# Optimization experiments

Hardware: AMD Instinct MI355X
Metric: run time of the kernel (lower is better)

The kernel has to match this reference:

```python
import jax, jax.numpy as jnp
import numpy as np


def setup_inputs() -> dict:
    key = jax.random.key(0)
    k1, k2 = jax.random.split(key)
    n, K = 1024, 8
    pred_y = jax.random.normal(k1, (n, K), dtype=jnp.float32)
    true_y = jax.random.randint(k2, (n, K), 0, 2).astype(jnp.int32)  # multi-label 0/1
    return {"pred_y": pred_y, "true_y": true_y}


def reference(pred_y, true_y):
    # mode == 'pairwise2':
    #   sum_{i,j} sum_{a: y[a,i]==1} sum_{b: y[b,j]==0} log(1 + exp(-(pred[a,i] - pred[b,j])))
    #   normalized by |S_pos| * |S_neg| (total counts over the whole label matrix).
    # The double class loop + cartesian_prod is exactly an all-pairs interaction
    # between flattened positive entries and flattened negative entries.
    pos = (true_y == 1)
    neg = (true_y == 0)
    v = pred_y.reshape(-1)                      # [n*K]
    mp = pos.reshape(-1).astype(pred_y.dtype)   # positive-entry mask
    mn = neg.reshape(-1).astype(pred_y.dtype)   # negative-entry mask
    # loss(p - q) = log(1 + exp(-(p - q))) = softplus(q - p)
    diff = v[None, :] - v[:, None]              # [nK, nK]; diff[a, b] = v_b - v_a
    sp = jax.nn.softplus(diff)
    total = jnp.sum(sp * (mp[:, None] * mn[None, :]))
    denom = jnp.sum(mp) * jnp.sum(mn)           # |S_pos| * |S_neg|
    return total / denom
```

## Files before the change

kernel.cpp:

```cpp
#include <hip/hip_runtime.h>

#define CBLK 256
#define GRID 1024
#define PBLK 512
#define RT   9

#define LOG2E 1.4426950408889634f
#define LN2   0.6931471805599453
#define BIGF  1.0e30f

__device__ __forceinline__ float fast_exp2(float x) {
#if __has_builtin(__builtin_amdgcn_exp2f)
    return __builtin_amdgcn_exp2f(x);
#else
    return exp2f(x);
#endif
}
__device__ __forceinline__ float fast_log2(float x) {
#if __has_builtin(__builtin_amdgcn_logf)
    return __builtin_amdgcn_logf(x);
#else
    return log2f(x);
#endif
}

__global__ void compact_kernel(const float* __restrict__ v,
                               const int* __restrict__ ty,
                               int* __restrict__ cnt,
                               float* __restrict__ vpos,
                               float* __restrict__ vneg,
                               int N) {
    const int i    = blockIdx.x * blockDim.x + threadIdx.x;
    const int lane = threadIdx.x & 63;

    const bool valid = (i < N);
    float val = 0.0f;
    int   t   = -1;
    if (valid) { val = v[i] * LOG2E; t = ty[i]; }

    const bool isP = valid && (t == 1);
    const bool isN = valid && (t == 0);

    const unsigned long long mp = __ballot(isP);
    const unsigned long long mn = __ballot(isN);
    const unsigned long long lt = (lane == 0) ? 0ull : (~0ull >> (64 - lane));

    int basep = 0, basen = 0;
    if (lane == 0) {
        basep = atomicAdd(&cnt[0], __popcll(mp));
        basen = atomicAdd(&cnt[1], __popcll(mn));
    }
    basep = __shfl(basep, 0, 64);
    basen = __shfl(basen, 0, 64);

    if (isP) vpos[basep + __popcll(mp & lt)] = val;
    if (isN) vneg[basen + __popcll(mn & lt)] = val;
}

__global__ __launch_bounds__(PBLK) void pair_kernel(
        const int* __restrict__ cnt,
        const float* __restrict__ vpos,
        const float* __restrict__ vneg,
        float* __restrict__ partials) {
    const int P   = cnt[0];
    const int Q   = cnt[1];
    const int tid = threadIdx.x;

    float accm = 0.0f;
    float accl = 0.0f;

    for (int base = 0; base < P; base += RT * PBLK) {
        float pa[RT];
        #pragma unroll
        for (int r = 0; r < RT; ++r) {
            const int idx = base + r * PBLK + tid;
            pa[r] = (idx < P) ? vpos[idx] : BIGF;
        }

        for (int b = blockIdx.x; b < Q; b += GRID) {
            const float vbl = vneg[b];
            float p = 1.0f;
            #pragma unroll
            for (int r = 0; r < RT; ++r) {
                const float x = vbl - pa[r];
                accm += fmaxf(x, 0.0f);
                const float e = fast_exp2(-fabsf(x));
                p = fmaf(p, e, p);
            }
            accl += fast_log2(p);
        }
    }

    float acc = accm + accl;

    for (int off = 32; off > 0; off >>= 1)
        acc += __shfl_down(acc, off, 64);

    __shared__ float wsum[PBLK / 64];
    const int lane = tid & 63;
    const int wid  = tid >> 6;
    if (lane == 0) wsum[wid] = acc;
    __syncthreads();
    if (tid == 0) {
        float s = 0.0f;
        #pragma unroll
        for (int wdx = 0; wdx < PBLK / 64; ++wdx) s += wsum[wdx];
        partials[blockIdx.x] = s;
    }
}

__global__ __launch_bounds__(256) void finalize_kernel(
        const float* __restrict__ partials, int nparts,
        const int* __restrict__ cnt,
        float* __restrict__ out) {
    const int tid = threadIdx.x;
    double s = 0.0;
    for (int k = tid; k < nparts; k += 256) s += (double)partials[k];

    __shared__ double sd[256];
    sd[tid] = s;
    __syncthreads();
    for (int off = 128; off > 0; off >>= 1) {
        if (tid < off) sd[tid] += sd[tid + off];
        __syncthreads();
    }
    if (tid == 0) {
        const double denom = (double)cnt[0] * (double)cnt[1];
        out[0] = (float)(sd[0] * LN2 / denom);
    }
}

extern "C" void kernel_launch(void* const* d_in, const int* in_sizes, int n_in,
                              void* d_out, int out_size, void* d_ws, size_t ws_size,
                              hipStream_t stream) {
    const float* v  = (const float*)d_in[0];
    const int*   ty = (const int*)d_in[1];
    float* out = (float*)d_out;
    const int N = in_sizes[0];

    char*  ws       = (char*)d_ws;
    int*   cnt      = (int*)ws;
    float* vpos     = (float*)(ws + 64);
    float* vneg     = vpos + N;
    float* partials = vneg + N;

    hipMemsetAsync(cnt, 0, 2 * sizeof(int), stream);

    const int cblocks = (N + CBLK - 1) / CBLK;
    compact_kernel<<<cblocks, CBLK, 0, stream>>>(v, ty, cnt, vpos, vneg, N);
    pair_kernel<<<GRID, PBLK, 0, stream>>>(cnt, vpos, vneg, partials);
    finalize_kernel<<<1, 256, 0, stream>>>(partials, GRID, cnt, out);
}
```

Baseline: 66.70 us.

## Fuse compaction into pair kernel via per-block LDS scan, drop memset

Each block now compacts the full label vector itself into shared memory with a wave/block prefix scan, placing positives at the front and negatives at the back. This removes the memset, the separate compaction kernel with its global atomics, and the global vpos/vneg round trip. The grid is reduced from 1024 to 256 blocks, so each block covers more negatives. In exchange every block redundantly reads all N inputs, N is capped at 8192 by the 32KB LDS buffer, and there is less parallelism for the pairwise work.

Measured after the change: 63.26 us. 5.2% less time.

```diff
diff --git a/kernel.cpp b/kernel.cpp
--- a/kernel.cpp
+++ b/kernel.cpp
@@ -1,9 +1,10 @@
 #include <hip/hip_runtime.h>
 
-#define CBLK 256
-#define GRID 1024
-#define PBLK 512
-#define RT   9
+#define GRID  256
+#define PBLK  512
+#define EPT   16
+#define RT    9
+#define NMAX  8192
 
 #define LOG2E 1.4426950408889634f
 #define LN2   0.6931471805599453
@@ -24,61 +25,95 @@
 #endif
 }
 
-__global__ void compact_kernel(const float* __restrict__ v,
-                               const int* __restrict__ ty,
-                               int* __restrict__ cnt,
-                               float* __restrict__ vpos,
-                               float* __restrict__ vneg,
-                               int N) {
-    const int i    = blockIdx.x * blockDim.x + threadIdx.x;
-    const int lane = threadIdx.x & 63;
+__global__ __launch_bounds__(PBLK) void fused_kernel(
+        const float* __restrict__ v,
+        const int*   __restrict__ ty,
+        int*         __restrict__ pcount,
+        float*       __restrict__ partials,
+        int N) {
+    __shared__ float buf[NMAX];
+    __shared__ int   wtot[PBLK / 64];
+    __shared__ float wsum[PBLK / 64];
 
-    const bool valid = (i < N);
-    float val = 0.0f;
-    int   t   = -1;
-    if (valid) { val = v[i] * LOG2E; t = ty[i]; }
+    const int tid  = threadIdx.x;
+    const int lane = tid & 63;
+    const int wid  = tid >> 6;
+    const int e0   = tid * EPT;
 
-    const bool isP = valid && (t == 1);
-    const bool isN = valid && (t == 0);
+    int pmask = 0;
+    if (e0 + EPT <= N) {
+        #pragma unroll
+        for (int j = 0; j < EPT / 4; ++j) {
+            const int4 t4 = *reinterpret_cast<const int4*>(ty + e0 + 4 * j);
+            pmask |= (t4.x == 1) << (4 * j + 0);
+            pmask |= (t4.y == 1) << (4 * j + 1);
+            pmask |= (t4.z == 1) << (4 * j + 2);
+            pmask |= (t4.w == 1) << (4 * j + 3);
+        }
+    } else {
+        for (int k = 0; k < EPT; ++k) {
+            const int i = e0 + k;
+            if (i < N && ty[i] == 1) pmask |= 1 << k;
+        }
+    }
+    const int cp = __popc(pmask);
 
-    const unsigned long long mp = __ballot(isP);
-    const unsigned long long mn = __ballot(isN);
-    const unsigned long long lt = (lane == 0) ? 0ull : (~0ull >> (64 - lane));
+    int scan = cp;
+    #pragma unroll
+    for (int off = 1; off < 64; off <<= 1) {
+        const int nb = __shfl_up(scan, off, 64);
+        if (lane >= off) scan += nb;
+    }
+    if (lane == 63) wtot[wid] = scan;
+    __syncthreads();
 
-    int basep = 0, basen = 0;
-    if (lane == 0) {
-        basep = atomicAdd(&cnt[0], __popcll(mp));
-        basen = atomicAdd(&cnt[1], __popcll(mn));
+    int waveBase = 0, P = 0;
+    #pragma unroll
+    for (int w = 0; w < PBLK / 64; ++w) {
+        const int t = wtot[w];
+        if (w < wid) waveBase += t;
+        P += t;
     }
-    basep = __shfl(basep, 0, 64);
-    basen = __shfl(basen, 0, 64);
+    const int elemsBefore = (e0 < N) ? e0 : N;
+    int pP = waveBase + scan - cp;
+    int pN = elemsBefore - pP;
+    const int Q = N - P;
 
-    if (isP) vpos[basep + __popcll(mp & lt)] = val;
-    if (isN) vneg[basen + __popcll(mn & lt)] = val;
-}
-
-__global__ __launch_bounds__(PBLK) void pair_kernel(
-        const int* __restrict__ cnt,
-        const float* __restrict__ vpos,
-        const float* __restrict__ vneg,
-        float* __restrict__ partials) {
-    const int P   = cnt[0];
-    const int Q   = cnt[1];
-    const int tid = threadIdx.x;
+    if (e0 + EPT <= N) {
+        #pragma unroll
+        for (int j = 0; j < EPT / 4; ++j) {
+            const float4 f4 = *reinterpret_cast<const float4*>(v + e0 + 4 * j);
+            const float vals[4] = {f4.x, f4.y, f4.z, f4.w};
+            #pragma unroll
+            for (int e = 0; e < 4; ++e) {
+                const float val = vals[e] * LOG2E;
+                if (pmask & (1 << (4 * j + e))) buf[pP++] = val;
+                else                            buf[N - 1 - (pN++)] = val;
+            }
+        }
+    } else {
+        for (int k = 0; k < EPT; ++k) {
+            const int i = e0 + k;
+            if (i < N) {
+                const float val = v[i] * LOG2E;
+                if (pmask & (1 << k)) buf[pP++] = val;
+                else                  buf[N - 1 - (pN++)] = val;
+            }
+        }
+    }
+    __syncthreads();
 
     float accm = 0.0f;
     float accl = 0.0f;
-
     for (int base = 0; base < P; base += RT * PBLK) {
         float pa[RT];
         #pragma unroll
         for (int r = 0; r < RT; ++r) {
             const int idx = base + r * PBLK + tid;
-            pa[r] = (idx < P) ? vpos[idx] : BIGF;
+            pa[r] = (idx < P) ? buf[idx] : BIGF;
         }
-
         for (int b = blockIdx.x; b < Q; b += GRID) {
-            const float vbl = vneg[b];
+            const float vbl = buf[N - 1 - b];
             float p = 1.0f;
             #pragma unroll
             for (int r = 0; r < RT; ++r) {
@@ -92,40 +127,36 @@
     }
 
     float acc = accm + accl;
-
+    #pragma unroll
     for (int off = 32; off > 0; off >>= 1)
         acc += __shfl_down(acc, off, 64);
-
-    __shared__ float wsum[PBLK / 64];
-    const int lane = tid & 63;
-    const int wid  = tid >> 6;
     if (lane == 0) wsum[wid] = acc;
     __syncthreads();
     if (tid == 0) {
         float s = 0.0f;
         #pragma unroll
-        for (int wdx = 0; wdx < PBLK / 64; ++wdx) s += wsum[wdx];
+        for (int w = 0; w < PBLK / 64; ++w) s += wsum[w];
         partials[blockIdx.x] = s;
+        if (blockIdx.x == 0) pcount[0] = P;
     }
 }
 
-__global__ __launch_bounds__(256) void finalize_kernel(
-        const float* __restrict__ partials, int nparts,
-        const int* __restrict__ cnt,
-        float* __restrict__ out) {
+__global__ __launch_bounds__(GRID) void finalize_kernel(
+        const float* __restrict__ partials,
+        const int*   __restrict__ pcount,
+        float*       __restrict__ out,
+        int N) {
     const int tid = threadIdx.x;
-    double s = 0.0;
-    for (int k = tid; k < nparts; k += 256) s += (double)partials[k];
-
-    __shared__ double sd[256];
-    sd[tid] = s;
+    __shared__ double sd[GRID];
+    sd[tid] = (double)partials[tid];
     __syncthreads();
-    for (int off = 128; off > 0; off >>= 1) {
+    for (int off = GRID / 2; off > 0; off >>= 1) {
         if (tid < off) sd[tid] += sd[tid + off];
         __syncthreads();
     }
     if (tid == 0) {
-        const double denom = (double)cnt[0] * (double)cnt[1];
+        const double P = (double)pcount[0];
+        const double denom = P * ((double)N - P);
         out[0] = (float)(sd[0] * LN2 / denom);
     }
 }
@@ -139,15 +170,9 @@
     const int N = in_sizes[0];
 
     char*  ws       = (char*)d_ws;
-    int*   cnt      = (int*)ws;
-    float* vpos     = (float*)(ws + 64);
-    float* vneg     = vpos + N;
-    float* partials = vneg + N;
+    int*   pcount   = (int*)ws;
+    float* partials = (float*)(ws + 64);
 
-    hipMemsetAsync(cnt, 0, 2 * sizeof(int), stream);
-
-    const int cblocks = (N + CBLK - 1) / CBLK;
-    compact_kernel<<<cblocks, CBLK, 0, stream>>>(v, ty, cnt, vpos, vneg, N);
-    pair_kernel<<<GRID, PBLK, 0, stream>>>(cnt, vpos, vneg, partials);
-    finalize_kernel<<<1, 256, 0, stream>>>(partials, GRID, cnt, out);
+    fused_kernel<<<GRID, PBLK, 0, stream>>>(v, ty, pcount, partials, N);
+    finalize_kernel<<<1, GRID, 0, stream>>>(partials, pcount, out, N);
 }
```
